# Kernel optimization log

Hardware: AMD Instinct MI355X
Metric: run time of the kernel (lower is better)

The kernel has to match this reference:

```python
import jax, jax.numpy as jnp
import numpy as np

H = 16          # nhead
N_LAYERS = 4    # stacks (weights are SHARED across stacks, as in the torch module)
PAD_IDX = 1
EPS = 1e-6
NEG = -1e9


def _pos_encoding(S, d):
    den = jnp.exp(-jnp.arange(0, d, 2, dtype=jnp.float32) * (np.log(10000.0) / d))
    ang = jnp.arange(S, dtype=jnp.float32)[:, None] * den[None, :]  # (S, d/2)
    pe = jnp.zeros((S, d), jnp.float32)
    pe = pe.at[:, 0::2].set(jnp.sin(ang)).at[:, 1::2].set(jnp.cos(ang))
    return pe


def _layer_norm(x, g, b):
    mu = jnp.mean(x, axis=-1, keepdims=True)
    var = jnp.mean((x - mu) ** 2, axis=-1, keepdims=True)
    return (x - mu) * jax.lax.rsqrt(var + EPS) * g + b


def _split_heads(x):
    B, S, d = x.shape
    return x.reshape(B, S, H, d // H).transpose(0, 2, 1, 3)  # (B,H,S,dk)


def _mha(q_in, k_in, v_in, mask, wq, bq, wk, bk, wv, bv, wo, bo):
    q = _split_heads(q_in @ wq + bq)
    k = _split_heads(k_in @ wk + bk)
    v = _split_heads(v_in @ wv + bv)
    dk = v.shape[-1]
    score = jnp.einsum('bhqd,bhkd->bhqk', q, k) / jnp.sqrt(jnp.float32(dk))
    if mask is not None:
        score = jnp.where(mask, score, NEG)
    p = jax.nn.softmax(score, axis=-1)
    out = jnp.einsum('bhqk,bhkd->bhqd', p, v)
    B, _, S, _ = out.shape
    out = out.transpose(0, 2, 1, 3).reshape(B, S, H * dk)
    return out @ wo + bo


def setup_inputs() -> dict:
    key = jax.random.key(0)
    B, St, Sm, d, dff, V = 4, 1024, 1024, 1024, 4096, 32000
    ks = jax.random.split(key, 32)
    sc = 1.0 / np.sqrt(d)
    inp = {
        'target_result': jax.random.randint(ks[0], (B, St), 0, V),
        'memory': jax.random.normal(ks[1], (B, Sm, d), jnp.float32),
        'emb': jax.random.normal(ks[2], (V, d), jnp.float32) * sc,
        'ff_w1': jax.random.normal(ks[3], (d, dff), jnp.float32) * sc,
        'ff_b1': jnp.zeros((dff,), jnp.float32),
        'ff_w2': jax.random.normal(ks[4], (dff, d), jnp.float32) / np.sqrt(dff),
        'ff_b2': jnp.zeros((d,), jnp.float32),
        'ln_g': jnp.ones((d,), jnp.float32),
        'ln_b': jnp.zeros((d,), jnp.float32),
    }
    i = 5
    for pre in ('sa', 'xa'):
        for nm in ('q', 'k', 'v', 'o'):
            inp[f'{pre}_w{nm}'] = jax.random.normal(ks[i], (d, d), jnp.float32) * sc
            inp[f'{pre}_b{nm}'] = jnp.zeros((d,), jnp.float32)
            i += 1
    return inp


def reference(target_result, memory, emb,
              sa_wq, sa_bq, sa_wk, sa_bk, sa_wv, sa_bv, sa_wo, sa_bo,
              xa_wq, xa_bq, xa_wk, xa_bk, xa_wv, xa_bv, xa_wo, xa_bo,
              ff_w1, ff_b1, ff_w2, ff_b2, ln_g, ln_b):
    B, St = target_result.shape
    d = emb.shape[1]
    # embed + scale + positional encoding (dropout = eval/identity)
    x = emb[target_result] * jnp.sqrt(jnp.float32(d)) + _pos_encoding(St, d)[None]
    # masks: pad mask (B,1,St,1) & causal (St,St) -> (B,1,St,St); source mask all-ones -> None
    pad = (target_result != PAD_IDX)[:, None, :, None]
    causal = jnp.tril(jnp.ones((St, St), bool))[None, None]
    tgt_mask = pad & causal
    out = x
    for _ in range(N_LAYERS):
        n = _layer_norm(out, ln_g, ln_b)
        out = out + _mha(n, n, n, tgt_mask,
                         sa_wq, sa_bq, sa_wk, sa_bk, sa_wv, sa_bv, sa_wo, sa_bo)
        n = _layer_norm(out, ln_g, ln_b)
        out = out + _mha(n, memory, memory, None,
                         xa_wq, xa_bq, xa_wk, xa_bk, xa_wv, xa_bv, xa_wo, xa_bo)
        n = _layer_norm(out, ln_g, ln_b)
        out = out + (jax.nn.relu(n @ ff_w1 + ff_b1) @ ff_w2 + ff_b2)
    return _layer_norm(out, ln_g, ln_b)
```

## Files before the change

kernel.cpp:

```cpp
#include <hip/hip_runtime.h>

typedef unsigned short u16;
typedef unsigned int u32;
typedef float f32x4 __attribute__((ext_vector_type(4)));
typedef float f32x16 __attribute__((ext_vector_type(16)));
typedef __bf16 bf16x8 __attribute__((ext_vector_type(8)));
typedef short short8 __attribute__((ext_vector_type(8)));
typedef u32 u32x4 __attribute__((ext_vector_type(4)));

#define DINLINE static __device__ __forceinline__

DINLINE u16 f2bf(float f) {
  u32 u = __builtin_bit_cast(u32, f);
  u += 0x7fffu + ((u >> 16) & 1u);
  return (u16)(u >> 16);
}

DINLINE float b2f(u32 lo16) {
  u32 u = lo16 << 16;
  return __builtin_bit_cast(float, u);
}

DINLINE f32x4 mfma16(short8 a, short8 b, f32x4 c) {
  return __builtin_amdgcn_mfma_f32_16x16x32_bf16(
      __builtin_bit_cast(bf16x8, a), __builtin_bit_cast(bf16x8, b), c, 0, 0, 0);
}

DINLINE f32x16 mfma32(short8 a, short8 b, f32x16 c) {
  return __builtin_amdgcn_mfma_f32_32x32x16_bf16(
      __builtin_bit_cast(bf16x8, a), __builtin_bit_cast(bf16x8, b), c, 0, 0, 0);
}

DINLINE u32 cvtpk(float lo, float hi) {
  u32 r;
  asm("v_cvt_pk_bf16_f32 %0, %1, %2" : "=v"(r) : "v"(lo), "v"(hi));
  return r;
}

DINLINE void plswap(u32& a, u32& b) {
  auto r = __builtin_amdgcn_permlane32_swap(a, b, false, false);
  a = (u32)r[0];
  b = (u32)r[1];
}

DINLINE void gld16(const void* g, void* l) {
  __builtin_amdgcn_global_load_lds(
      (const __attribute__((address_space(1))) void*)g,
      (__attribute__((address_space(3))) void*)l, 16, 0, 0);
}

__global__ __launch_bounds__(256) void transpose_wt(const float* __restrict__ src,
                                                    u16* __restrict__ dst, int K, int N,
                                                    float scale) {
  __shared__ float tile[32][33];
  int n0 = blockIdx.x * 32, k0 = blockIdx.y * 32;
  int tx = threadIdx.x, ty = threadIdx.y;
#pragma unroll
  for (int j = 0; j < 32; j += 8)
    tile[ty + j][tx] = src[(size_t)(k0 + ty + j) * N + n0 + tx];
  __syncthreads();
#pragma unroll
  for (int j = 0; j < 32; j += 8)
    dst[(size_t)(n0 + ty + j) * K + k0 + tx] = f2bf(tile[tx][ty + j] * scale);
}

__global__ __launch_bounds__(256) void cvt_bf16(const float* __restrict__ src,
                                                u16* __restrict__ dst) {
  size_t i = (size_t)blockIdx.x * 256 + threadIdx.x;
  float4 v = ((const float4*)src)[i];
  u32 lo = (u32)f2bf(v.x) | ((u32)f2bf(v.y) << 16);
  u32 hi = (u32)f2bf(v.z) | ((u32)f2bf(v.w) << 16);
  uint2 o; o.x = lo; o.y = hi;
  ((uint2*)dst)[i] = o;
}

__global__ void concat3(const float* __restrict__ a, const float* __restrict__ b,
                        const float* __restrict__ c, float* __restrict__ o, float sa) {
  int i = blockIdx.x * 256 + threadIdx.x;
  float v = (i < 1024) ? a[i] * sa : (i < 2048 ? b[i - 1024] : c[i - 2048]);
  o[i] = v;
}

__global__ void scale_vec(const float* __restrict__ a, float* __restrict__ o, float s) {
  int i = blockIdx.x * 256 + threadIdx.x;
  o[i] = a[i] * s;
}

__global__ __launch_bounds__(256) void pe_k(float* __restrict__ pe) {
  int s = blockIdx.x;
  for (int c = threadIdx.x; c < 1024; c += 256) {
    int i = c >> 1;
    float den = expf(-(float)(2 * i) * 0.0089944739960705f);
    float ang = (float)s * den;
    pe[s * 1024 + c] = (c & 1) ? cosf(ang) : sinf(ang);
  }
}

__global__ __launch_bounds__(256) void embed_pe(const int* __restrict__ tgt,
                                                const float* __restrict__ emb,
                                                const float* __restrict__ pe,
                                                float* __restrict__ x,
                                                u16* __restrict__ xbf) {
  int row = blockIdx.x;
  int s = row & 1023;
  int tok = tgt[row];
  float4 e = ((const float4*)(emb + (size_t)tok * 1024))[threadIdx.x];
  float4 p = ((const float4*)(pe + (size_t)s * 1024))[threadIdx.x];
  float4 o;
  o.x = e.x * 32.0f + p.x; o.y = e.y * 32.0f + p.y;
  o.z = e.z * 32.0f + p.z; o.w = e.w * 32.0f + p.w;
  ((float4*)(x + (size_t)row * 1024))[threadIdx.x] = o;
  ushort4 ob;
  ob.x = f2bf(o.x); ob.y = f2bf(o.y); ob.z = f2bf(o.z); ob.w = f2bf(o.w);
  ((ushort4*)(xbf + (size_t)row * 1024))[threadIdx.x] = ob;
}

template <int MODE>
__global__ __launch_bounds__(256) void ln_k(const float* __restrict__ Xf,
                                            const u16* __restrict__ Xb,
                                            const float* __restrict__ g,
                                            const float* __restrict__ bta,
                                            u16* __restrict__ obf,
                                            float* __restrict__ of) {
  int row = blockIdx.x;
  int t = threadIdx.x;
  float v0, v1, v2, v3;
  if (MODE == 1) {
    float4 v = ((const float4*)(Xf + (size_t)row * 1024))[t];
    v0 = v.x; v1 = v.y; v2 = v.z; v3 = v.w;
  } else {
    uint2 p2 = ((const uint2*)(Xb + (size_t)row * 1024))[t];
    v0 = b2f(p2.x); v1 = b2f(p2.x >> 16); v2 = b2f(p2.y); v3 = b2f(p2.y >> 16);
  }
  float s = v0 + v1 + v2 + v3;
  float sq = v0 * v0 + v1 * v1 + v2 * v2 + v3 * v3;
#pragma unroll
  for (int o = 1; o < 64; o <<= 1) {
    s += __shfl_xor(s, o);
    sq += __shfl_xor(sq, o);
  }
  __shared__ float red[8];
  int wid = t >> 6;
  if ((t & 63) == 0) { red[wid * 2] = s; red[wid * 2 + 1] = sq; }
  __syncthreads();
  s = red[0] + red[2] + red[4] + red[6];
  sq = red[1] + red[3] + red[5] + red[7];
  float mean = s * (1.0f / 1024.0f);
  float var = sq * (1.0f / 1024.0f) - mean * mean;
  float rstd = rsqrtf(var + 1e-6f);
  float4 gv = ((const float4*)g)[t];
  float4 bv = ((const float4*)bta)[t];
  float y0 = (v0 - mean) * rstd * gv.x + bv.x;
  float y1 = (v1 - mean) * rstd * gv.y + bv.y;
  float y2 = (v2 - mean) * rstd * gv.z + bv.z;
  float y3 = (v3 - mean) * rstd * gv.w + bv.w;
  if (MODE == 1) {
    float4 o4; o4.x = y0; o4.y = y1; o4.z = y2; o4.w = y3;
    ((float4*)of)[(size_t)row * 256 + t] = o4;
  } else {
    u32 lo = (u32)f2bf(y0) | ((u32)f2bf(y1) << 16);
    u32 hi = (u32)f2bf(y2) | ((u32)f2bf(y3) << 16);
    uint2 o2; o2.x = lo; o2.y = hi;
    ((uint2*)obf)[(size_t)row * 256 + t] = o2;
  }
}

template <int BM, int EPI>
__global__ __launch_bounds__(256) void gemm2(
    const u16* __restrict__ A, const u16* __restrict__ Bt,
    const float* __restrict__ bias, float* __restrict__ X,
    u16* __restrict__ Cbf, int N, int K) {
  constexpr int ABYT = BM * 128;
  constexpr int BBYT = 128 * 128;
  constexpr int MF = BM / 32;
  __shared__ __align__(16) char smem[2 * (ABYT + BBYT)];

  const int tid = threadIdx.x;
  const int w = tid >> 6, l = tid & 63;
  const int lg = l >> 4, lc = l & 15;
  const int m0 = blockIdx.y * BM, n0 = blockIdx.x * 128;
  const int wr = w >> 1, wc = w & 1;
  const char* Ab = (const char*)A;
  const char* Bb = (const char*)Bt;
  const size_t sA = (size_t)K * 2;

  f32x4 acc[MF][4];
  const f32x4 zv = {0.f, 0.f, 0.f, 0.f};
#pragma unroll
  for (int m = 0; m < MF; ++m)
#pragma unroll
    for (int n = 0; n < 4; ++n) acc[m][n] = zv;

  const int srow = l >> 3;
  const int scol = ((l & 7) ^ srow) << 4;

  auto stage = [&](char* bufA, char* bufB, int kt) {
    const size_t kb = (size_t)kt << 7;
#pragma unroll
    for (int i = 0; i < BM / 32; ++i) {
      const int r = i * 32 + w * 8 + srow;
      gld16(Ab + (size_t)(m0 + r) * sA + kb + scol, bufA + (i * 4 + w) * 1024 + l * 16);
    }
#pragma unroll
    for (int i = 0; i < 4; ++i) {
      const int r = i * 32 + w * 8 + srow;
      gld16(Bb + (size_t)(n0 + r) * sA + kb + scol, bufB + (i * 4 + w) * 1024 + l * 16);
    }
  };

  stage(smem, smem + ABYT, 0);
  __syncthreads();

  const int nkt = K >> 6;
  int cur = 0;
  for (int kt = 0; kt < nkt; ++kt) {
    char* As = smem + cur * (ABYT + BBYT);
    char* Bs = As + ABYT;
    if (kt + 1 < nkt) {
      char* An = smem + (cur ^ 1) * (ABYT + BBYT);
      stage(An, An + ABYT, kt + 1);
    }
    __builtin_amdgcn_s_setprio(1);
#pragma unroll
    for (int ks = 0; ks < 2; ++ks) {
      short8 af[MF], bf4[4];
#pragma unroll
      for (int m = 0; m < MF; ++m) {
        int row = wr * (BM / 2) + m * 16 + lc;
        int col = (ks * 64 + (lg << 4)) ^ ((row & 7) << 4);
        af[m] = *(const short8*)(As + row * 128 + col);
      }
#pragma unroll
      for (int n = 0; n < 4; ++n) {
        int row = wc * 64 + n * 16 + lc;
        int col = (ks * 64 + (lg << 4)) ^ ((row & 7) << 4);
        bf4[n] = *(const short8*)(Bs + row * 128 + col);
      }
#pragma unroll
      for (int m = 0; m < MF; ++m)
#pragma unroll
        for (int n = 0; n < 4; ++n) acc[m][n] = mfma16(af[m], bf4[n], acc[m][n]);
    }
    __builtin_amdgcn_s_setprio(0);
    __syncthreads();
    cur ^= 1;
  }

  float bv[4];
#pragma unroll
  for (int n = 0; n < 4; ++n) bv[n] = bias[n0 + wc * 64 + n * 16 + lc];

  if (EPI <= 1) {
    u16* ct = (u16*)smem;
#pragma unroll
    for (int m = 0; m < MF; ++m)
#pragma unroll
      for (int n = 0; n < 4; ++n)
#pragma unroll
        for (int r = 0; r < 4; ++r) {
          int row = wr * (BM / 2) + m * 16 + (lg << 2) + r;
          int col = wc * 64 + n * 16 + lc;
          float v = acc[m][n][r] + bv[n];
          if (EPI == 1) v = v > 0.f ? v : 0.f;
          ct[row * 136 + col] = f2bf(v);
        }
    __syncthreads();
#pragma unroll
    for (int j = 0; j < BM / 16; ++j) {
      int c = j * 256 + tid;
      int row = c >> 4, colb = (c & 15) * 8;
      *(short8*)(Cbf + (size_t)(m0 + row) * N + n0 + colb) =
          *(const short8*)(ct + row * 136 + colb);
    }
  } else if (EPI == 2) {
    float* cf = (float*)smem;
#pragma unroll
    for (int m = 0; m < MF; ++m)
#pragma unroll
      for (int n = 0; n < 4; ++n)
#pragma unroll
        for (int r = 0; r < 4; ++r) {
          int row = wr * (BM / 2) + m * 16 + (lg << 2) + r;
          int col = wc * 64 + n * 16 + lc;
          cf[row * 128 + col] = acc[m][n][r] + bv[n];
        }
    __syncthreads();
#pragma unroll
    for (int j = 0; j < BM / 8; ++j) {
      int c = j * 256 + tid;
      int row = c >> 5, colb = (c & 31) * 4;
      size_t idx = (size_t)(m0 + row) * N + n0 + colb;
      float4 s4 = *(const float4*)(cf + row * 128 + colb);
      float4 xv = *(const float4*)(X + idx);
      xv.x += s4.x; xv.y += s4.y; xv.z += s4.z; xv.w += s4.w;
      *(float4*)(X + idx) = xv;
      ushort4 ob;
      ob.x = f2bf(xv.x); ob.y = f2bf(xv.y); ob.z = f2bf(xv.z); ob.w = f2bf(xv.w);
      *(ushort4*)(Cbf + idx) = ob;
    }
  } else {
    u16* ct = (u16*)smem;
#pragma unroll
    for (int m = 0; m < MF; ++m)
#pragma unroll
      for (int n = 0; n < 4; ++n)
#pragma unroll
        for (int r = 0; r < 4; ++r) {
          int row = wr * (BM / 2) + m * 16 + (lg << 2) + r;
          int col = wc * 64 + n * 16 + lc;
          ct[col * 136 + row] = f2bf(acc[m][n][r] + bv[n]);
        }
    __syncthreads();
    const int bb = m0 >> 10, ms = m0 & 1023;
#pragma unroll
    for (int j = 0; j < BM / 16; ++j) {
      int flat = j * 256 + tid;
      int sb = flat & (BM / 8 - 1);
      int col = flat / (BM / 8);
      int n = n0 + col;
      u16* dst = Cbf + (size_t)(((bb << 4) + (n >> 6)) * 64 + (n & 63)) * 1024 + ms + sb * 8;
      *(short8*)dst = *(const short8*)(ct + col * 136 + sb * 8);
    }
  }
}

template <bool CAUSAL>
__global__ __launch_bounds__(256) void attn_lds(
    const u16* __restrict__ Qp, int sQ, const u16* __restrict__ Kp, int sK,
    const u16* __restrict__ Vt, const int* __restrict__ tgt,
    u16* __restrict__ Out) {
  __shared__ __align__(16) char smem[2][32768];
  const int tid = threadIdx.x;
  const int w = tid >> 6, l = tid & 63;
  const int bh = blockIdx.x & 63, sub = blockIdx.x >> 6;
  const int b = bh >> 4, h = bh & 15;
  const int lq = l & 31, hi = l >> 5;
  const int qt = sub * 4 + w;
  const int q0 = qt * 32;

  const char* Kc = (const char*)(Kp + (size_t)b * 1024 * sK + h * 64);
  const char* Vc = (const char*)(Vt + (size_t)bh * 64 * 1024);
  const u16* Qh = Qp + (size_t)b * 1024 * sQ + h * 64;

  short8 qb[4];
  {
    const u16* qrow = Qh + (size_t)(q0 + lq) * sQ + hi * 8;
#pragma unroll
    for (int c = 0; c < 4; ++c) qb[c] = *(const short8*)(qrow + c * 16);
  }

  bool row_ok = true;
  int my_nkt = 16;
  int blk_nst = CAUSAL ? (sub + 1) : 8;
  if (CAUSAL) {
    row_ok = (tgt[b * 1024 + q0 + lq] != 1);
    bool anypad_w = __any(!row_ok);
    __shared__ int s_pad;
    if (tid == 0) s_pad = 0;
    __syncthreads();
    if (anypad_w && l == 0) s_pad = 1;
    __syncthreads();
    if (s_pad) { my_nkt = 16; blk_nst = 8; }
    else my_nkt = (qt >> 1) + 1;
  }

  const int srow = l >> 3;
  const int scol = ((l & 7) ^ srow) << 4;
  auto stage = [&](int buf, int st) {
    const int k0 = st * 128;
    char* Ks = smem[buf];
    char* Vs = smem[buf] + 16384;
#pragma unroll
    for (int t2 = 0; t2 < 2; ++t2)
#pragma unroll
      for (int i = 0; i < 2; ++i) {
        const int r = i * 32 + w * 8 + srow;
        gld16(Kc + (size_t)(k0 + t2 * 64 + r) * sK * 2 + scol, Ks + t2 * 8192 + r * 128);
        gld16(Vc + (size_t)r * 2048 + (size_t)(k0 + t2 * 64) * 2 + scol,
              Vs + t2 * 8192 + r * 128);
      }
  };

  float m = -3.0e38f, lsum = 0.f;
  f32x16 oacc[2];
#pragma unroll
  for (int r = 0; r < 16; ++r) { oacc[0][r] = 0.f; oacc[1][r] = 0.f; }

  stage(0, 0);
  __syncthreads();
  int cur = 0;

  for (int st = 0; st < blk_nst; ++st) {
    if (st + 1 < blk_nst) stage(cur ^ 1, st + 1);
#pragma unroll
    for (int t2 = 0; t2 < 2; ++t2) {
      const int t64 = st * 2 + t2;
      if (t64 < my_nkt) {
        const char* Ks = smem[cur] + t2 * 8192;
        const char* Vs = smem[cur] + 16384 + t2 * 8192;
        const int k0 = t64 * 64;
        f32x16 stt[2];
        __builtin_amdgcn_s_setprio(1);
#pragma unroll
        for (int s = 0; s < 2; ++s) {
          const int row = s * 32 + lq;
          const int swz = (row & 7) << 4;
          f32x16 a;
#pragma unroll
          for (int r = 0; r < 16; ++r) a[r] = 0.f;
#pragma unroll
          for (int c = 0; c < 4; ++c) {
            short8 kb = *(const short8*)(Ks + row * 128 + ((c * 32 + hi * 16) ^ swz));
            a = mfma32(kb, qb[c], a);
          }
          stt[s] = a;
        }
        __builtin_amdgcn_s_setprio(0);
        if (CAUSAL) {
#pragma unroll
          for (int s = 0; s < 2; ++s) {
            if (!row_ok || (k0 + s * 32 + 31 > q0)) {
#pragma unroll
              for (int r = 0; r < 16; ++r) {
                int kg = k0 + s * 32 + (r & 3) + 8 * (r >> 2) + 4 * hi;
                bool ok = row_ok && (kg <= q0 + lq);
                if (!ok) stt[s][r] = -1e9f;
              }
            }
          }
        }
        float tm;
        {
          float v[16];
#pragma unroll
          for (int r = 0; r < 16; ++r) v[r] = fmaxf(stt[0][r], stt[1][r]);
#pragma unroll
          for (int w2 = 8; w2 >= 1; w2 >>= 1)
#pragma unroll
            for (int r = 0; r < w2; ++r) v[r] = fmaxf(v[r], v[r + w2]);
          tm = v[0];
        }
        tm = fmaxf(tm, __shfl_xor(tm, 32));
        if (!__all(tm <= m + 8.0f)) {
          float mn = fmaxf(m, tm);
          float alpha = __expf(m - mn);
          lsum *= alpha;
          m = mn;
#pragma unroll
          for (int r = 0; r < 16; ++r) {
            int crow = (r & 3) + 8 * (r >> 2) + 4 * hi;
            float av = __shfl(alpha, crow);
            oacc[0][r] *= av;
            oacc[1][r] *= av;
          }
        }
        float tsa0 = 0.f, tsa1 = 0.f, tsa2 = 0.f, tsa3 = 0.f;
#pragma unroll
        for (int s = 0; s < 2; ++s) {
#pragma unroll
          for (int r = 0; r < 16; ++r) {
            float e = __expf(stt[s][r] - m);
            stt[s][r] = e;
            if ((r & 3) == 0) tsa0 += e;
            else if ((r & 3) == 1) tsa1 += e;
            else if ((r & 3) == 2) tsa2 += e;
            else tsa3 += e;
          }
        }
        float ts = (tsa0 + tsa1) + (tsa2 + tsa3);
        ts += __shfl_xor(ts, 32);
        lsum += ts;
        short8 pa[4];
#pragma unroll
        for (int s = 0; s < 2; ++s) {
          u32 cc[8];
#pragma unroll
          for (int t = 0; t < 4; ++t) {
            cc[2 * t]     = cvtpk(stt[s][4 * t + 0], stt[s][4 * t + 1]);
            cc[2 * t + 1] = cvtpk(stt[s][4 * t + 2], stt[s][4 * t + 3]);
          }
          plswap(cc[0], cc[2]);
          plswap(cc[1], cc[3]);
          plswap(cc[4], cc[6]);
          plswap(cc[5], cc[7]);
          u32x4 w0 = {cc[0], cc[1], cc[2], cc[3]};
          u32x4 w1 = {cc[4], cc[5], cc[6], cc[7]};
          pa[2 * s]     = __builtin_bit_cast(short8, w0);
          pa[2 * s + 1] = __builtin_bit_cast(short8, w1);
        }
        __builtin_amdgcn_s_setprio(1);
#pragma unroll
        for (int dt = 0; dt < 2; ++dt) {
          const int row = dt * 32 + lq;
          const int swz = (row & 7) << 4;
#pragma unroll
          for (int c = 0; c < 4; ++c) {
            short8 vb = *(const short8*)(Vs + row * 128 + ((c * 32 + hi * 16) ^ swz));
            oacc[dt] = mfma32(pa[c], vb, oacc[dt]);
          }
        }
        __builtin_amdgcn_s_setprio(0);
      }
    }
    __syncthreads();
    cur ^= 1;
  }

#pragma unroll
  for (int r = 0; r < 16; ++r) {
    int crow = (r & 3) + 8 * (r >> 2) + 4 * hi;
    float lv = __shfl(lsum, crow);
    float linv = 1.0f / lv;
    int qg = q0 + crow;
    size_t base = ((size_t)b * 1024 + qg) * 1024 + h * 64 + lq;
    Out[base] = f2bf(oacc[0][r] * linv);
    Out[base + 32] = f2bf(oacc[1][r] * linv);
  }
}

extern "C" void kernel_launch(void* const* d_in, const int* in_sizes, int n_in,
                              void* d_out, int out_size, void* d_ws, size_t ws_size,
                              hipStream_t stream) {
  const int* tgt = (const int*)d_in[0];
  const float* memory = (const float*)d_in[1];
  const float* emb = (const float*)d_in[2];
  const float* ff_w1 = (const float*)d_in[3];
  const float* ff_b1 = (const float*)d_in[4];
  const float* ff_w2 = (const float*)d_in[5];
  const float* ff_b2 = (const float*)d_in[6];
  const float* ln_g = (const float*)d_in[7];
  const float* ln_b = (const float*)d_in[8];
  const float* sa_wq = (const float*)d_in[9];
  const float* sa_bq = (const float*)d_in[10];
  const float* sa_wk = (const float*)d_in[11];
  const float* sa_bk = (const float*)d_in[12];
  const float* sa_wv = (const float*)d_in[13];
  const float* sa_bv = (const float*)d_in[14];
  const float* sa_wo = (const float*)d_in[15];
  const float* sa_bo = (const float*)d_in[16];
  const float* xa_wq = (const float*)d_in[17];
  const float* xa_bq = (const float*)d_in[18];
  const float* xa_wk = (const float*)d_in[19];
  const float* xa_bk = (const float*)d_in[20];
  const float* xa_wv = (const float*)d_in[21];
  const float* xa_bv = (const float*)d_in[22];
  const float* xa_wo = (const float*)d_in[23];
  const float* xa_bo = (const float*)d_in[24];

  char* ws = (char*)d_ws;
  size_t off = 0;
  auto alloc = [&](size_t bytes) {
    char* p = ws + off;
    off += (bytes + 255) & ~(size_t)255;
    return p;
  };
  float* x   = (float*)alloc(4096ull * 1024 * 4);
  u16* xbf   = (u16*)alloc(4096ull * 1024 * 2);
  u16* nbf   = (u16*)alloc(4096ull * 1024 * 2);
  u16* qkv   = (u16*)alloc(4096ull * 2048 * 2);
  u16* q2    = (u16*)alloc(4096ull * 1024 * 2);
  u16* attn  = (u16*)alloc(4096ull * 1024 * 2);
  u16* vt    = (u16*)alloc(64ull * 64 * 1024 * 2);
  u16* kx    = (u16*)alloc(4096ull * 1024 * 2);
  u16* vtx   = (u16*)alloc(64ull * 64 * 1024 * 2);
  u16* h1    = (u16*)alloc(4096ull * 4096 * 2);
  u16* memb  = (u16*)alloc(4096ull * 1024 * 2);
  u16* w_qkv = (u16*)alloc(3072ull * 1024 * 2);
  u16* w_sao = (u16*)alloc(1024ull * 1024 * 2);
  u16* w_xaq = (u16*)alloc(1024ull * 1024 * 2);
  u16* w_xak = (u16*)alloc(1024ull * 1024 * 2);
  u16* w_xav = (u16*)alloc(1024ull * 1024 * 2);
  u16* w_xao = (u16*)alloc(1024ull * 1024 * 2);
  u16* w_ff1 = (u16*)alloc(4096ull * 1024 * 2);
  u16* w_ff2 = (u16*)alloc(1024ull * 4096 * 2);
  float* b_qkv = (float*)alloc(3072 * 4);
  float* b_xaq = (float*)alloc(1024 * 4);
  float* pe    = (float*)alloc(1024ull * 1024 * 4);

  dim3 blk(256);
  dim3 b32(32, 8);
  const float QS = 0.125f;

  transpose_wt<<<dim3(32, 32), b32, 0, stream>>>(sa_wq, w_qkv, 1024, 1024, QS);
  transpose_wt<<<dim3(32, 32), b32, 0, stream>>>(sa_wk, w_qkv + 1024 * 1024, 1024, 1024, 1.f);
  transpose_wt<<<dim3(32, 32), b32, 0, stream>>>(sa_wv, w_qkv + 2048 * 1024, 1024, 1024, 1.f);
  transpose_wt<<<dim3(32, 32), b32, 0, stream>>>(sa_wo, w_sao, 1024, 1024, 1.f);
  transpose_wt<<<dim3(32, 32), b32, 0, stream>>>(xa_wq, w_xaq, 1024, 1024, QS);
  transpose_wt<<<dim3(32, 32), b32, 0, stream>>>(xa_wk, w_xak, 1024, 1024, 1.f);
  transpose_wt<<<dim3(32, 32), b32, 0, stream>>>(xa_wv, w_xav, 1024, 1024, 1.f);
  transpose_wt<<<dim3(32, 32), b32, 0, stream>>>(xa_wo, w_xao, 1024, 1024, 1.f);
  transpose_wt<<<dim3(128, 32), b32, 0, stream>>>(ff_w1, w_ff1, 1024, 4096, 1.f);
  transpose_wt<<<dim3(32, 128), b32, 0, stream>>>(ff_w2, w_ff2, 4096, 1024, 1.f);
  concat3<<<12, blk, 0, stream>>>(sa_bq, sa_bk, sa_bv, b_qkv, QS);
  scale_vec<<<4, blk, 0, stream>>>(xa_bq, b_xaq, QS);
  cvt_bf16<<<4096, blk, 0, stream>>>(memory, memb);
  pe_k<<<1024, blk, 0, stream>>>(pe);
  embed_pe<<<4096, blk, 0, stream>>>(tgt, emb, pe, x, xbf);

  gemm2<64, 0><<<dim3(8, 64), blk, 0, stream>>>(memb, w_xak, xa_bk, nullptr, kx, 1024, 1024);
  gemm2<64, 3><<<dim3(8, 64), blk, 0, stream>>>(memb, w_xav, xa_bv, nullptr, vtx, 1024, 1024);

  for (int layer = 0; layer < 4; ++layer) {
    ln_k<2><<<4096, blk, 0, stream>>>(nullptr, xbf, ln_g, ln_b, nbf, nullptr);
    gemm2<128, 0><<<dim3(16, 32), blk, 0, stream>>>(nbf, w_qkv, b_qkv, nullptr, qkv, 2048, 1024);
    gemm2<64, 3><<<dim3(8, 64), blk, 0, stream>>>(nbf, w_qkv + 2048 * 1024, b_qkv + 2048,
                                                  nullptr, vt, 1024, 1024);
    attn_lds<true><<<512, blk, 0, stream>>>(qkv, 2048, qkv + 1024, 2048, vt, tgt, attn);
    gemm2<64, 2><<<dim3(8, 64), blk, 0, stream>>>(attn, w_sao, sa_bo, x, xbf, 1024, 1024);
    ln_k<2><<<4096, blk, 0, stream>>>(nullptr, xbf, ln_g, ln_b, nbf, nullptr);
    gemm2<64, 0><<<dim3(8, 64), blk, 0, stream>>>(nbf, w_xaq, b_xaq, nullptr, q2, 1024, 1024);
    attn_lds<false><<<512, blk, 0, stream>>>(q2, 1024, kx, 1024, vtx, nullptr, attn);
    gemm2<64, 2><<<dim3(8, 64), blk, 0, stream>>>(attn, w_xao, xa_bo, x, xbf, 1024, 1024);
    ln_k<2><<<4096, blk, 0, stream>>>(nullptr, xbf, ln_g, ln_b, nbf, nullptr);
    gemm2<128, 1><<<dim3(32, 32), blk, 0, stream>>>(nbf, w_ff1, ff_b1, nullptr, h1, 4096, 1024);
    gemm2<64, 2><<<dim3(8, 64), blk, 0, stream>>>(h1, w_ff2, ff_b2, x, xbf, 1024, 4096);
  }
  ln_k<1><<<4096, blk, 0, stream>>>(x, nullptr, ln_g, ln_b, nullptr, (float*)d_out);
}
```

Before: 1.136 ms.

## Load GEMM B operand directly from global into registers, staging only A in LDS

The GEMM kernel no longer stages the weight (B) tile through shared memory. Each wave loads its B fragments straight from global memory into registers, double-buffered across two k-steps, while A keeps its LDS double buffer. The loop is unrolled by two, and launch bounds now request two blocks per SM. This cuts LDS footprint and LDS traffic so occupancy can rise, at the cost of uncoalesced 16-byte global loads for B, more register pressure, and B data being fetched redundantly by the two wave rows.

```diff
diff --git a/kernel.cpp b/kernel.cpp
--- a/kernel.cpp
+++ b/kernel.cpp
@@ -166,14 +166,15 @@
 }
 
 template <int BM, int EPI>
-__global__ __launch_bounds__(256) void gemm2(
+__global__ __launch_bounds__(256, 2) void gemm2g(
     const u16* __restrict__ A, const u16* __restrict__ Bt,
     const float* __restrict__ bias, float* __restrict__ X,
     u16* __restrict__ Cbf, int N, int K) {
   constexpr int ABYT = BM * 128;
-  constexpr int BBYT = 128 * 128;
   constexpr int MF = BM / 32;
-  __shared__ __align__(16) char smem[2 * (ABYT + BBYT)];
+  constexpr int EPIB = (EPI == 2) ? BM * 512 : 34816;
+  constexpr int SMEM = (2 * ABYT > EPIB) ? 2 * ABYT : EPIB;
+  __shared__ __align__(16) char smem[SMEM];
 
   const int tid = threadIdx.x;
   const int w = tid >> 6, l = tid & 63;
@@ -181,7 +182,6 @@
   const int m0 = blockIdx.y * BM, n0 = blockIdx.x * 128;
   const int wr = w >> 1, wc = w & 1;
   const char* Ab = (const char*)A;
-  const char* Bb = (const char*)Bt;
   const size_t sA = (size_t)K * 2;
 
   f32x4 acc[MF][4];
@@ -194,36 +194,30 @@
   const int srow = l >> 3;
   const int scol = ((l & 7) ^ srow) << 4;
 
-  auto stage = [&](char* bufA, char* bufB, int kt) {
+  auto stageA = [&](char* bufA, int kt) {
     const size_t kb = (size_t)kt << 7;
 #pragma unroll
     for (int i = 0; i < BM / 32; ++i) {
       const int r = i * 32 + w * 8 + srow;
       gld16(Ab + (size_t)(m0 + r) * sA + kb + scol, bufA + (i * 4 + w) * 1024 + l * 16);
     }
-#pragma unroll
-    for (int i = 0; i < 4; ++i) {
-      const int r = i * 32 + w * 8 + srow;
-      gld16(Bb + (size_t)(n0 + r) * sA + kb + scol, bufB + (i * 4 + w) * 1024 + l * 16);
-    }
   };
 
-  stage(smem, smem + ABYT, 0);
-  __syncthreads();
-
-  const int nkt = K >> 6;
-  int cur = 0;
-  for (int kt = 0; kt < nkt; ++kt) {
-    char* As = smem + cur * (ABYT + BBYT);
-    char* Bs = As + ABYT;
-    if (kt + 1 < nkt) {
-      char* An = smem + (cur ^ 1) * (ABYT + BBYT);
-      stage(An, An + ABYT, kt + 1);
-    }
-    __builtin_amdgcn_s_setprio(1);
+  auto loadB = [&](short8 (&bd)[2][4], int kt) {
+#pragma unroll
+    for (int ks = 0; ks < 2; ++ks)
+#pragma unroll
+      for (int n = 0; n < 4; ++n) {
+        const u16* p = Bt + (size_t)(n0 + wc * 64 + n * 16 + lc) * K +
+                       kt * 64 + ks * 32 + lg * 8;
+        bd[ks][n] = *(const short8*)p;
+      }
+  };
+
+  auto compute = [&](const char* As, short8 (&bc)[2][4]) {
 #pragma unroll
     for (int ks = 0; ks < 2; ++ks) {
-      short8 af[MF], bf4[4];
+      short8 af[MF];
 #pragma unroll
       for (int m = 0; m < MF; ++m) {
         int row = wr * (BM / 2) + m * 16 + lc;
@@ -231,19 +225,37 @@
         af[m] = *(const short8*)(As + row * 128 + col);
       }
 #pragma unroll
-      for (int n = 0; n < 4; ++n) {
-        int row = wc * 64 + n * 16 + lc;
-        int col = (ks * 64 + (lg << 4)) ^ ((row & 7) << 4);
-        bf4[n] = *(const short8*)(Bs + row * 128 + col);
+      for (int m = 0; m < MF; ++m)
+#pragma unroll
+        for (int n = 0; n < 4; ++n) acc[m][n] = mfma16(af[m], bc[ks][n], acc[m][n]);
+    }
+  };
+
+  short8 bA[2][4], bB[2][4];
+  stageA(smem, 0);
+  loadB(bA, 0);
+  __syncthreads();
+
+  const int nkt = K >> 6;
+  for (int kt = 0; kt < nkt; kt += 2) {
+    {
+      stageA(smem + ABYT, kt + 1);
+      loadB(bB, kt + 1);
+      __builtin_amdgcn_s_setprio(1);
+      compute(smem, bA);
+      __builtin_amdgcn_s_setprio(0);
+      __syncthreads();
+    }
+    {
+      if (kt + 2 < nkt) {
+        stageA(smem, kt + 2);
+        loadB(bA, kt + 2);
       }
-#pragma unroll
-      for (int m = 0; m < MF; ++m)
-#pragma unroll
-        for (int n = 0; n < 4; ++n) acc[m][n] = mfma16(af[m], bf4[n], acc[m][n]);
-    }
-    __builtin_amdgcn_s_setprio(0);
-    __syncthreads();
-    cur ^= 1;
+      __builtin_amdgcn_s_setprio(1);
+      compute(smem + ABYT, bB);
+      __builtin_amdgcn_s_setprio(0);
+      __syncthreads();
+    }
   }
 
   float bv[4];
@@ -597,23 +609,23 @@
   pe_k<<<1024, blk, 0, stream>>>(pe);
   embed_pe<<<4096, blk, 0, stream>>>(tgt, emb, pe, x, xbf);
 
-  gemm2<64, 0><<<dim3(8, 64), blk, 0, stream>>>(memb, w_xak, xa_bk, nullptr, kx, 1024, 1024);
-  gemm2<64, 3><<<dim3(8, 64), blk, 0, stream>>>(memb, w_xav, xa_bv, nullptr, vtx, 1024, 1024);
+  gemm2g<64, 0><<<dim3(8, 64), blk, 0, stream>>>(memb, w_xak, xa_bk, nullptr, kx, 1024, 1024);
+  gemm2g<64, 3><<<dim3(8, 64), blk, 0, stream>>>(memb, w_xav, xa_bv, nullptr, vtx, 1024, 1024);
 
   for (int layer = 0; layer < 4; ++layer) {
     ln_k<2><<<4096, blk, 0, stream>>>(nullptr, xbf, ln_g, ln_b, nbf, nullptr);
-    gemm2<128, 0><<<dim3(16, 32), blk, 0, stream>>>(nbf, w_qkv, b_qkv, nullptr, qkv, 2048, 1024);
-    gemm2<64, 3><<<dim3(8, 64), blk, 0, stream>>>(nbf, w_qkv + 2048 * 1024, b_qkv + 2048,
-                                                  nullptr, vt, 1024, 1024);
+    gemm2g<128, 0><<<dim3(16, 32), blk, 0, stream>>>(nbf, w_qkv, b_qkv, nullptr, qkv, 2048, 1024);
+    gemm2g<64, 3><<<dim3(8, 64), blk, 0, stream>>>(nbf, w_qkv + 2048 * 1024, b_qkv + 2048,
+                                                   nullptr, vt, 1024, 1024);
     attn_lds<true><<<512, blk, 0, stream>>>(qkv, 2048, qkv + 1024, 2048, vt, tgt, attn);
-    gemm2<64, 2><<<dim3(8, 64), blk, 0, stream>>>(attn, w_sao, sa_bo, x, xbf, 1024, 1024);
+    gemm2g<64, 2><<<dim3(8, 64), blk, 0, stream>>>(attn, w_sao, sa_bo, x, xbf, 1024, 1024);
     ln_k<2><<<4096, blk, 0, stream>>>(nullptr, xbf, ln_g, ln_b, nbf, nullptr);
-    gemm2<64, 0><<<dim3(8, 64), blk, 0, stream>>>(nbf, w_xaq, b_xaq, nullptr, q2, 1024, 1024);
+    gemm2g<64, 0><<<dim3(8, 64), blk, 0, stream>>>(nbf, w_xaq, b_xaq, nullptr, q2, 1024, 1024);
     attn_lds<false><<<512, blk, 0, stream>>>(q2, 1024, kx, 1024, vtx, nullptr, attn);
-    gemm2<64, 2><<<dim3(8, 64), blk, 0, stream>>>(attn, w_xao, xa_bo, x, xbf, 1024, 1024);
+    gemm2g<64, 2><<<dim3(8, 64), blk, 0, stream>>>(attn, w_xao, xa_bo, x, xbf, 1024, 1024);
     ln_k<2><<<4096, blk, 0, stream>>>(nullptr, xbf, ln_g, ln_b, nbf, nullptr);
-    gemm2<128, 1><<<dim3(32, 32), blk, 0, stream>>>(nbf, w_ff1, ff_b1, nullptr, h1, 4096, 1024);
-    gemm2<64, 2><<<dim3(8, 64), blk, 0, stream>>>(h1, w_ff2, ff_b2, x, xbf, 1024, 4096);
+    gemm2g<128, 1><<<dim3(32, 32), blk, 0, stream>>>(nbf, w_ff1, ff_b1, nullptr, h1, 4096, 1024);
+    gemm2g<64, 2><<<dim3(8, 64), blk, 0, stream>>>(h1, w_ff2, ff_b2, x, xbf, 1024, 4096);
   }
   ln_k<1><<<4096, blk, 0, stream>>>(x, nullptr, ln_g, ln_b, nullptr, (float*)d_out);
 }
```

Result: slower. 2.250 ms (+98.0%).
